# Kernel tuning notes

Measured on AMD Instinct MI355X. Metric: run time of the kernel, lower is better.

## Reference

```python
import jax, jax.numpy as jnp
import numpy as np

N, D, H, E, K, C = 8192, 1024, 2048, 8, 2, 2560  # tokens, d_model, hidden, experts, top_k, capacity


def setup_inputs() -> dict:
    key = jax.random.key(0)
    ks = jax.random.split(key, 8)
    s_in, s_h = 1.0 / np.sqrt(D), 1.0 / np.sqrt(H)
    return {
        "x": jax.random.normal(ks[0], (N, D), jnp.float32),
        "Wg": jax.random.uniform(ks[1], (D, E), jnp.float32, -s_in, s_in),
        "bg": jnp.zeros((E,), jnp.float32),
        "W1": jax.random.uniform(ks[2], (E, D, H), jnp.float32, -s_in, s_in),
        "b1": jnp.zeros((E, H), jnp.float32),
        "W2": jax.random.uniform(ks[3], (E, H, H), jnp.float32, -s_h, s_h),
        "b2": jnp.zeros((E, H), jnp.float32),
    }


def reference(x, Wg, bg, W1, b1, W2, b2):
    n = x.shape[0]
    logits = x @ Wg + bg                                  # [N, E]
    probs = jax.nn.softmax(logits, axis=-1)
    topk_probs, topk_idx = jax.lax.top_k(probs, K)        # [N, K]

    # auxiliary losses (training mode)
    importance = probs.sum(0)
    importance_loss = jnp.var(importance) / (E ** 2)
    rows = jnp.arange(n)[:, None]
    mask = jnp.zeros_like(probs).at[rows, topk_idx].set(1.0)
    routing_probs = probs * mask
    expert_usage = mask.mean(0)
    routing_weights = routing_probs.mean(0)
    load_balance_loss = E * (expert_usage * routing_weights).sum()
    aux_loss = importance_loss + load_balance_loss

    # dispatch: rank of each (token, k) slot within its expert, in flat order
    flat_e = topk_idx.reshape(-1)                          # [N*K]
    flat_p = topk_probs.reshape(-1)                        # [N*K]
    sample_idx = jnp.repeat(jnp.arange(n), K)              # [N*K]
    oh = (flat_e[:, None] == jnp.arange(E)[None, :]).astype(jnp.int32)  # [N*K, E]
    rank = jnp.take_along_axis(jnp.cumsum(oh, axis=0), flat_e[:, None], axis=1)[:, 0] - 1
    keep = rank < C                                        # capacity truncation (first-come)
    r_safe = jnp.where(keep, rank, C)                      # C is out-of-bounds -> dropped

    buf = jnp.zeros((E, C, D), x.dtype).at[flat_e, r_safe].set(x[sample_idx], mode="drop")
    h = jax.nn.gelu(jnp.einsum("ecd,edh->ech", buf, W1) + b1[:, None, :], approximate=False)
    y = jnp.einsum("ech,eho->eco", h, W2) + b2[:, None, :]  # [E, C, H]

    gathered = y[flat_e, jnp.minimum(r_safe, C - 1)]       # [N*K, H]
    weighted = gathered * (flat_p * keep.astype(x.dtype))[:, None]
    outputs = jnp.zeros((n, H), x.dtype).at[sample_idx].add(weighted)
    return outputs, aux_loss
```

## Files before the change

### kernel.cpp

```cpp
#include <hip/hip_runtime.h>
#include <math.h>
#include <stdint.h>

#define N_TOK 8192
#define DMODEL 1024
#define HID 2048
#define NEXP 8
#define TOPK 2
#define CAP 2560
#define NTALL 1408

typedef __bf16 bf16x8 __attribute__((ext_vector_type(8)));
typedef float f32x4 __attribute__((ext_vector_type(4)));
typedef unsigned int u32x4 __attribute__((ext_vector_type(4)));

__device__ __forceinline__ unsigned short f2b(float f) {
    unsigned int u = __builtin_bit_cast(unsigned int, f);
    u += 0x7fffu + ((u >> 16) & 1u);
    return (unsigned short)(u >> 16);
}
__device__ __forceinline__ float b2f(unsigned short s) {
    unsigned int u = ((unsigned int)s) << 16;
    return __builtin_bit_cast(float, u);
}

__device__ __forceinline__ float gelu_f(float v) {
    const float ax = fabsf(v) * 0.70710678118654752440f;
    const float t = __builtin_amdgcn_rcpf(1.f + 0.3275911f * ax);
    float poly = ((((1.061405429f * t - 1.453152027f) * t + 1.421413741f) * t
                   - 0.284496736f) * t + 0.254829592f) * t;
    float er = 1.f - poly * __expf(-ax * ax);
    er = (v >= 0.f) ? er : -er;
    return 0.5f * v * (1.f + er);
}

__device__ __forceinline__ void gload_lds16(const void* g, void* lds) {
    __builtin_amdgcn_global_load_lds(
        (const __attribute__((address_space(1))) unsigned int*)(uintptr_t)g,
        (__attribute__((address_space(3))) unsigned int*)(unsigned int)(uintptr_t)lds,
        16, 0, 0);
}

__global__ __launch_bounds__(256) void gate_kernel(
    const float* __restrict__ x, const float* __restrict__ Wg,
    const float* __restrict__ bg,
    int* __restrict__ flat_e, float* __restrict__ flat_p,
    float* __restrict__ imp_part, float* __restrict__ sel_part,
    unsigned short* __restrict__ xbf)
{
    __shared__ float s_imp[4][NEXP];
    __shared__ float s_sel[4][NEXP];
    const int wave = threadIdx.x >> 6;
    const int lane = threadIdx.x & 63;
    const int t = blockIdx.x * 4 + wave;

    float acc[NEXP];
#pragma unroll
    for (int e = 0; e < NEXP; ++e) acc[e] = 0.f;
    const float* xr = x + (size_t)t * DMODEL;
    unsigned short* xbr = xbf + (size_t)t * DMODEL;
    for (int d = lane; d < DMODEL; d += 64) {
        const float xv = xr[d];
        xbr[d] = f2b(xv);
#pragma unroll
        for (int e = 0; e < NEXP; ++e) acc[e] += xv * Wg[d * NEXP + e];
    }
#pragma unroll
    for (int off = 32; off > 0; off >>= 1) {
#pragma unroll
        for (int e = 0; e < NEXP; ++e) acc[e] += __shfl_xor(acc[e], off);
    }
    float lg[NEXP], mx = -1e30f;
#pragma unroll
    for (int e = 0; e < NEXP; ++e) { lg[e] = acc[e] + bg[e]; mx = fmaxf(mx, lg[e]); }
    float p[NEXP], s = 0.f;
#pragma unroll
    for (int e = 0; e < NEXP; ++e) { p[e] = expf(lg[e] - mx); s += p[e]; }
    const float inv = 1.f / s;
#pragma unroll
    for (int e = 0; e < NEXP; ++e) p[e] *= inv;

    int i0 = 0;
#pragma unroll
    for (int e = 1; e < NEXP; ++e) if (p[e] > p[i0]) i0 = e;
    int i1 = (i0 == 0) ? 1 : 0;
#pragma unroll
    for (int e = 0; e < NEXP; ++e) if (e != i0 && p[e] > p[i1]) i1 = e;

    if (lane == 0) {
        flat_e[2 * t] = i0;  flat_e[2 * t + 1] = i1;
        flat_p[2 * t] = p[i0]; flat_p[2 * t + 1] = p[i1];
#pragma unroll
        for (int e = 0; e < NEXP; ++e) {
            s_imp[wave][e] = p[e];
            s_sel[wave][e] = (e == i0) ? p[i0] : ((e == i1) ? p[i1] : 0.f);
        }
    }
    __syncthreads();
    if (threadIdx.x < NEXP) {
        const int e = threadIdx.x;
        float a = 0.f, b = 0.f;
#pragma unroll
        for (int w = 0; w < 4; ++w) { a += s_imp[w][e]; b += s_sel[w][e]; }
        imp_part[blockIdx.x * NEXP + e] = a;
        sel_part[blockIdx.x * NEXP + e] = b;
    }
}

__global__ __launch_bounds__(1024) void scan_kernel(
    const int* __restrict__ flat_e, int* __restrict__ slot_rank,
    int* __restrict__ row_token, int* __restrict__ n_kept,
    int* __restrict__ cnt_full, unsigned short* __restrict__ xbf_pad,
    int* __restrict__ ctrs)
{
    __shared__ int wave_tot[16][NEXP];
    __shared__ int base[NEXP];
    const int tid = threadIdx.x, lane = tid & 63, w = tid >> 6;
    if (tid < NEXP) base[tid] = 0;
    if (tid < 209) ctrs[tid] = 0;
    for (int i = tid; i < DMODEL; i += 1024) xbf_pad[i] = 0;
    __syncthreads();
    const unsigned long long ltmask =
        (lane == 0) ? 0ull : (~0ull >> (64 - lane));
    for (int chunk = 0; chunk < (N_TOK * TOPK) / 1024; ++chunk) {
        const int s = chunk * 1024 + tid;
        const int e = flat_e[s];
        int prefix = 0;
#pragma unroll
        for (int ee = 0; ee < NEXP; ++ee) {
            unsigned long long m = __ballot(e == ee);
            if (ee == e) prefix = __popcll(m & ltmask);
            if (lane == 0) wave_tot[w][ee] = __popcll(m);
        }
        __syncthreads();
        int before = base[e];
        for (int ww = 0; ww < w; ++ww) before += wave_tot[ww][e];
        const int rank = before + prefix;
        slot_rank[s] = rank;
        if (rank < CAP) row_token[e * CAP + rank] = s >> 1;
        __syncthreads();
        if (tid < NEXP) {
            int add = 0;
#pragma unroll
            for (int ww = 0; ww < 16; ++ww) add += wave_tot[ww][tid];
            base[tid] += add;
        }
        __syncthreads();
    }
    for (int i = tid; i < NEXP * CAP; i += 1024) {
        const int ee = i / CAP;
        const int r = i - ee * CAP;
        const int ne = base[ee] < CAP ? base[ee] : CAP;
        if (r >= ne) row_token[i] = N_TOK;
    }
    if (tid < NEXP) {
        n_kept[tid] = min(base[tid], CAP);
        cnt_full[tid] = base[tid];
    }
}

#define VMGATE4() do { asm volatile("s_waitcnt vmcnt(4)" ::: "memory"); \
                       __builtin_amdgcn_sched_barrier(0); } while (0)
#define VMGATE0() do { asm volatile("s_waitcnt vmcnt(0)" ::: "memory"); \
                       __builtin_amdgcn_sched_barrier(0); } while (0)
#define NOGATE() ((void)0)

#define PHASE(mf0, STAGE_STMT, TAIL_STMT) do {                                   \
    bf16x8 a0 = lda(c, (mf0), 0), a1 = lda(c, (mf0), 1);                         \
    bf16x8 a2 = lda(c, (mf0) + 1, 0), a3 = lda(c, (mf0) + 1, 1);                 \
    STAGE_STMT;                                                                  \
    __builtin_amdgcn_s_barrier();                                                \
    asm volatile("s_waitcnt lgkmcnt(0)" ::: "memory");                           \
    __builtin_amdgcn_sched_barrier(0);                                           \
    __builtin_amdgcn_s_setprio(1);                                               \
    _Pragma("unroll")                                                            \
    for (int nf = 0; nf < 4; ++nf) {                                             \
        acc[(mf0)][nf] = __builtin_amdgcn_mfma_f32_16x16x32_bf16(                \
            a0, bfr[nf][0], acc[(mf0)][nf], 0, 0, 0);                            \
        acc[(mf0)][nf] = __builtin_amdgcn_mfma_f32_16x16x32_bf16(                \
            a1, bfr[nf][1], acc[(mf0)][nf], 0, 0, 0);                            \
        acc[(mf0) + 1][nf] = __builtin_amdgcn_mfma_f32_16x16x32_bf16(            \
            a2, bfr[nf][0], acc[(mf0) + 1][nf], 0, 0, 0);                        \
        acc[(mf0) + 1][nf] = __builtin_amdgcn_mfma_f32_16x16x32_bf16(            \
            a3, bfr[nf][1], acc[(mf0) + 1][nf], 0, 0, 0);                        \
    }                                                                            \
    __builtin_amdgcn_s_setprio(0);                                               \
    TAIL_STMT;                                                                   \
    __builtin_amdgcn_s_barrier();                                                \
} while (0)

__global__ __launch_bounds__(512, 1) void mfma_fused(
    const unsigned short* __restrict__ xbf,
    const float* __restrict__ W1,
    const float* __restrict__ W2,
    unsigned short* w1t,
    unsigned short* w2t,
    const float* __restrict__ b1, const float* __restrict__ b2,
    unsigned short* hbuf,
    unsigned short* __restrict__ ybuf,
    const int* __restrict__ row_token, const int* __restrict__ n_kept,
    int* __restrict__ ctr)
{
    __shared__ unsigned short smem[81920];
    int* s_item = (int*)((char*)smem + 163836);
    int* hdone  = ctr + 1;
    int* w1flag = ctr + 81;
    int* w2flag = ctr + 145;

    const int t = threadIdx.x;
    const int w = t >> 6, lane = t & 63;
    const int wm = w >> 2, wn = w & 3;
    const int l15 = lane & 15, lq = lane >> 4;
    const int srow_lo = t >> 3;

    const int sx = (l15 & 4) << 3;
    const int kbx0 = (lq * 16) ^ sx;
    const int kbx1 = (64 + lq * 16) ^ sx;
    auto lda = [&](int cbuf, int mf, int ks) -> bf16x8 {
        return *(const bf16x8*)((const char*)smem + cbuf * 32768 +
                                (wm * 128 + mf * 16 + l15) * 128 + (ks ? kbx1 : kbx0));
    };
    auto ldb = [&](int cbuf, int nf, int ks) -> bf16x8 {
        return *(const bf16x8*)((const char*)smem + 65536 + cbuf * 32768 +
                                (wn * 64 + nf * 16 + l15) * 128 + (ks ? kbx1 : kbx0));
    };

    for (;;) {
        __syncthreads();
        if (t == 0) *s_item = atomicAdd(ctr, 1);
        __syncthreads();
        const int item = *s_item;
        if (item >= NTALL) break;

        bool isT = false, isW2 = false;
        int tIdx = 0, gIdx = 0;
        bool g2 = false;
        if (item < 64)        { isT = true; isW2 = false; tIdx = item; }
        else if (item < 128)  { gIdx = item - 64;  g2 = false; }
        else if (item < 192)  { isT = true; isW2 = true; tIdx = item - 128; }
        else if (item < 768)  { gIdx = item - 128; g2 = false; }
        else                  { gIdx = item - 768; g2 = true; }

        if (isT) {
            const int e = tIdx >> 3, n = tIdx & 7;
            const int R = isW2 ? HID : DMODEL;
            const float* Wsrc = (isW2 ? W2 : W1) + (size_t)e * R * HID + n * 256;
            unsigned short* Wdst =
                (isW2 ? w2t : w1t) + ((size_t)e * HID + n * 256) * R;
            unsigned short (*ts)[66] = (unsigned short(*)[66])smem;
            const int lr = t >> 6, lc = t & 63;
            const int cc = t >> 3, rq = (t & 7) * 8;
            for (int kb = 0; kb < R; kb += 64) {
                for (int nb = 0; nb < 4; ++nb) {
                    __syncthreads();
#pragma unroll
                    for (int i = 0; i < 8; ++i)
                        ts[lr + i * 8][lc] = f2b(__builtin_nontemporal_load(
                            &Wsrc[(size_t)(kb + lr + i * 8) * HID + nb * 64 + lc]));
                    __syncthreads();
                    unsigned short v[8];
#pragma unroll
                    for (int k2 = 0; k2 < 8; ++k2) v[k2] = ts[rq + k2][cc];
                    u32x4 o;
                    o[0] = v[0] | ((unsigned)v[1] << 16);
                    o[1] = v[2] | ((unsigned)v[3] << 16);
                    o[2] = v[4] | ((unsigned)v[5] << 16);
                    o[3] = v[6] | ((unsigned)v[7] << 16);
                    *(u32x4*)&Wdst[(size_t)(nb * 64 + cc) * R + kb + rq] = o;
                }
            }
            __syncthreads();
            if (t == 0)
                __hip_atomic_fetch_add(&(isW2 ? w2flag : w1flag)[tIdx], 1,
                                       __ATOMIC_RELEASE, __HIP_MEMORY_SCOPE_AGENT);
            continue;
        }

        const int e = gIdx / 80;
        const int rem = gIdx - e * 80;
        const int m = rem % 10;
        const int n = rem / 10;
        const int m0 = m * 256, n0 = n * 256;
        if (m0 >= n_kept[e]) continue;

        if (t == 0) {
            int* wf = g2 ? &w2flag[e * 8 + n] : &w1flag[e * 8 + n];
            while (__hip_atomic_load(wf, __ATOMIC_ACQUIRE,
                                     __HIP_MEMORY_SCOPE_AGENT) < 1)
                __builtin_amdgcn_s_sleep(8);
            if (g2) {
                while (__hip_atomic_load(&hdone[e * 10 + m], __ATOMIC_ACQUIRE,
                                         __HIP_MEMORY_SCOPE_AGENT) < 8)
                    __builtin_amdgcn_s_sleep(8);
            }
        }
        __syncthreads();

        const int Kdim = g2 ? HID : DMODEL;
        const int NT = Kdim >> 6;
        const unsigned short* A  = g2 ? hbuf : xbf;
        const unsigned short* Wt = g2 ? w2t : w1t;

        long abase[2][2], bbase[2][2];
#pragma unroll
        for (int h = 0; h < 2; ++h) {
#pragma unroll
            for (int cc2 = 0; cc2 < 2; ++cc2) {
                const int srow = h * 128 + cc2 * 64 + srow_lo;
                const int skoff = ((t & 7) * 8) ^ ((srow & 4) << 2);
                long ar;
                if (g2) ar = ((long)e * CAP + m0 + srow) * (long)Kdim;
                else    ar = (long)row_token[e * CAP + m0 + srow] * Kdim;
                abase[h][cc2] = ar + skoff;
                bbase[h][cc2] = ((long)e * HID + n0 + srow) * (long)Kdim + skoff;
            }
        }
        auto stageA = [&](int buf, int h0, int ktile) {
            const long ko = (long)ktile * 64;
            char* base = (char*)smem + buf * 32768 + h0 * 16384 + w * 1024;
            gload_lds16(A + (h0 ? abase[1][0] : abase[0][0]) + ko, base);
            gload_lds16(A + (h0 ? abase[1][1] : abase[0][1]) + ko, base + 8192);
        };
        auto stageB = [&](int buf, int h0, int ktile) {
            const long ko = (long)ktile * 64;
            char* base = (char*)smem + 65536 + buf * 32768 + h0 * 16384 + w * 1024;
            gload_lds16(Wt + (h0 ? bbase[1][0] : bbase[0][0]) + ko, base);
            gload_lds16(Wt + (h0 ? bbase[1][1] : bbase[0][1]) + ko, base + 8192);
        };

        f32x4 acc[8][4];
#pragma unroll
        for (int mm = 0; mm < 8; ++mm)
#pragma unroll
            for (int nn = 0; nn < 4; ++nn) acc[mm][nn] = (f32x4)0.f;

        stageA(0, 0, 0); stageA(0, 1, 0);
        stageB(0, 0, 0); stageB(0, 1, 0);
        stageB(1, 0, 1); stageB(1, 1, 1);
        VMGATE4();
        __builtin_amdgcn_s_barrier();

        int bcur = 0;
        for (int kt = 0; kt < NT; ++kt) {
            const int c = kt & 1, o = c ^ 1;
            const int ktA = kt + 1;
            const int ktB = kt + 2;
            int bst = bcur + 2; if (bst >= 3) bst -= 3;

            bf16x8 bfr[4][2];
#pragma unroll
            for (int nf = 0; nf < 4; ++nf) {
                bfr[nf][0] = ldb(bcur, nf, 0);
                bfr[nf][1] = ldb(bcur, nf, 1);
            }
            PHASE(0, if (ktA < NT) stageA(o, 0, ktA), NOGATE());
            PHASE(2, if (ktA < NT) stageA(o, 1, ktA), NOGATE());
            PHASE(4, if (ktB < NT) stageB(bst, 0, ktB), NOGATE());
            if (ktB < NT) {
                PHASE(6, stageB(bst, 1, ktB), VMGATE4());
            } else {
                PHASE(6, NOGATE(), VMGATE0());
            }
            bcur = (bcur == 2) ? 0 : bcur + 1;
        }

        const float* be = (g2 ? b2 : b1) + (size_t)e * HID;
        unsigned short* outp = g2 ? ybuf : hbuf;
        float bv[4];
#pragma unroll
        for (int nf = 0; nf < 4; ++nf)
            bv[nf] = be[n0 + wn * 64 + nf * 16 + l15];
#pragma unroll
        for (int mf = 0; mf < 8; ++mf) {
#pragma unroll
            for (int j = 0; j < 4; ++j) {
                const int row = m0 + wm * 128 + mf * 16 + lq * 4 + j;
                unsigned short* orow =
                    outp + ((size_t)e * CAP + row) * HID + n0 + wn * 64 + l15;
#pragma unroll
                for (int nf = 0; nf < 4; ++nf) {
                    float v = acc[mf][nf][j] + bv[nf];
                    if (!g2) {
                        v = gelu_f(v);
                        orow[nf * 16] = f2b(v);
                    } else {
                        __builtin_nontemporal_store(f2b(v), &orow[nf * 16]);
                    }
                }
            }
        }

        if (!g2) {
            __syncthreads();
            if (t == 0)
                __hip_atomic_fetch_add(&hdone[e * 10 + m], 1, __ATOMIC_RELEASE,
                                       __HIP_MEMORY_SCOPE_AGENT);
        }
    }
}

__global__ __launch_bounds__(256) void combine_kernel(
    const unsigned short* __restrict__ y, const int* __restrict__ flat_e,
    const float* __restrict__ flat_p, const int* __restrict__ slot_rank,
    float* __restrict__ out)
{
    const int t = blockIdx.x;
    const int e0 = flat_e[2 * t], e1 = flat_e[2 * t + 1];
    const int r0 = slot_rank[2 * t], r1 = slot_rank[2 * t + 1];
    const bool k0 = r0 < CAP, k1 = r1 < CAP;
    const float w0 = k0 ? flat_p[2 * t] : 0.f;
    const float w1 = k1 ? flat_p[2 * t + 1] : 0.f;
    const unsigned short* y0 = y + ((size_t)e0 * CAP + (k0 ? r0 : 0)) * HID;
    const unsigned short* y1 = y + ((size_t)e1 * CAP + (k1 ? r1 : 0)) * HID;
    float* orow = out + (size_t)t * HID;
    const int c = threadIdx.x * 8;
    u32x4 av = k0 ? __builtin_nontemporal_load((const u32x4*)(y0 + c)) : (u32x4)0u;
    u32x4 bv = k1 ? __builtin_nontemporal_load((const u32x4*)(y1 + c)) : (u32x4)0u;
    float o[8];
    auto comb2 = [&](unsigned int a, unsigned int b, float* dst) {
        dst[0] = w0 * b2f((unsigned short)(a & 0xffffu)) +
                 w1 * b2f((unsigned short)(b & 0xffffu));
        dst[1] = w0 * b2f((unsigned short)(a >> 16)) +
                 w1 * b2f((unsigned short)(b >> 16));
    };
    comb2(av[0], bv[0], o + 0); comb2(av[1], bv[1], o + 2);
    comb2(av[2], bv[2], o + 4); comb2(av[3], bv[3], o + 6);
    f32x4 o0 = {o[0], o[1], o[2], o[3]};
    f32x4 o1 = {o[4], o[5], o[6], o[7]};
    __builtin_nontemporal_store(o0, (f32x4*)(orow + c));
    __builtin_nontemporal_store(o1, (f32x4*)(orow + c + 4));
}

__global__ __launch_bounds__(64) void aux_kernel(
    const float* __restrict__ imp_part, const float* __restrict__ sel_part,
    const int* __restrict__ cnt_full, float* __restrict__ out_aux,
    const int nparts)
{
    const int lane = threadIdx.x;
    __shared__ float imp_s[NEXP], sel_s[NEXP];
    for (int e = 0; e < NEXP; ++e) {
        float a = 0.f, b = 0.f;
        for (int i = lane; i < nparts; i += 64) {
            a += imp_part[i * NEXP + e];
            b += sel_part[i * NEXP + e];
        }
#pragma unroll
        for (int off = 32; off > 0; off >>= 1) {
            a += __shfl_xor(a, off);
            b += __shfl_xor(b, off);
        }
        if (lane == 0) { imp_s[e] = a; sel_s[e] = b; }
    }
    __syncthreads();
    if (lane == 0) {
        double mean = 0.0;
        for (int e = 0; e < NEXP; ++e) mean += imp_s[e];
        mean /= NEXP;
        double var = 0.0;
        for (int e = 0; e < NEXP; ++e) {
            const double d = (double)imp_s[e] - mean;
            var += d * d;
        }
        var /= NEXP;
        double load = 0.0;
        for (int e = 0; e < NEXP; ++e)
            load += ((double)cnt_full[e] / N_TOK) * ((double)sel_s[e] / N_TOK);
        load *= NEXP;
        out_aux[0] = (float)(var / (NEXP * NEXP) + load);
    }
}

extern "C" void kernel_launch(void* const* d_in, const int* in_sizes, int n_in,
                              void* d_out, int out_size, void* d_ws, size_t ws_size,
                              hipStream_t stream) {
    const float* x  = (const float*)d_in[0];
    const float* Wg = (const float*)d_in[1];
    const float* bg = (const float*)d_in[2];
    const float* W1 = (const float*)d_in[3];
    const float* b1 = (const float*)d_in[4];
    const float* W2 = (const float*)d_in[5];
    const float* b2 = (const float*)d_in[6];
    float* out = (float*)d_out;
    (void)in_sizes; (void)n_in; (void)out_size; (void)ws_size;

    char* ws = (char*)d_ws;
    size_t off = 0;
    auto alloc = [&](size_t bytes) -> void* {
        void* p = ws + off;
        off = (off + bytes + 255) & ~(size_t)255;
        return p;
    };
    int*   n_kept    = (int*)alloc(NEXP * sizeof(int));
    int*   cnt_full  = (int*)alloc(NEXP * sizeof(int));
    int*   ctrs      = (int*)alloc(209 * sizeof(int));
    int*   flat_e    = (int*)alloc((size_t)N_TOK * TOPK * sizeof(int));
    float* flat_p    = (float*)alloc((size_t)N_TOK * TOPK * sizeof(float));
    int*   slot_rank = (int*)alloc((size_t)N_TOK * TOPK * sizeof(int));
    int*   row_tok   = (int*)alloc((size_t)NEXP * CAP * sizeof(int));
    float* imp_part  = (float*)alloc((size_t)(N_TOK / 4) * NEXP * sizeof(float));
    float* sel_part  = (float*)alloc((size_t)(N_TOK / 4) * NEXP * sizeof(float));
    unsigned short* xbf  = (unsigned short*)alloc((size_t)(N_TOK + 1) * DMODEL * 2);
    unsigned short* w1t  = (unsigned short*)alloc((size_t)NEXP * DMODEL * HID * 2);
    unsigned short* w2t  = (unsigned short*)alloc((size_t)NEXP * HID * HID * 2);
    unsigned short* hbuf = (unsigned short*)alloc((size_t)NEXP * CAP * HID * 2);
    unsigned short* ybuf = (unsigned short*)alloc((size_t)NEXP * CAP * HID * 2);

    gate_kernel<<<N_TOK / 4, 256, 0, stream>>>(x, Wg, bg, flat_e, flat_p,
                                               imp_part, sel_part, xbf);
    scan_kernel<<<1, 1024, 0, stream>>>(flat_e, slot_rank, row_tok, n_kept,
                                        cnt_full, xbf + (size_t)N_TOK * DMODEL,
                                        ctrs);

    mfma_fused<<<256, 512, 0, stream>>>(xbf, W1, W2, w1t, w2t, b1, b2,
                                        hbuf, ybuf, row_tok, n_kept, ctrs);

    combine_kernel<<<N_TOK, 256, 0, stream>>>(ybuf, flat_e, flat_p, slot_rank, out);
    aux_kernel<<<1, 64, 0, stream>>>(imp_part, sel_part, cnt_full,
                                     out + (size_t)N_TOK * HID, N_TOK / 4);
}
```

Measured before the change: 526.7 us.

## Move W1 transpose-convert into a separate kernel before the fused GEMM

The W1 fp32-to-bf16 transpose now runs in a dedicated grid-wide kernel instead of as work items inside the persistent fused GEMM kernel. GEMM1 items no longer spin on per-tile W1 flags, and the work-item list and counter array shrink to match. The W2 transpose stays in-kernel and is still overlapped with GEMM1. The trade is an extra launch plus a serial dependency, in exchange for a fully parallel transpose and no per-tile polling. The final output stores also switch from nontemporal to normal stores.

```diff
diff --git a/kernel.cpp b/kernel.cpp
--- a/kernel.cpp
+++ b/kernel.cpp
@@ -8,7 +8,7 @@
 #define NEXP 8
 #define TOPK 2
 #define CAP 2560
-#define NTALL 1408
+#define NTALL 1344
 
 typedef __bf16 bf16x8 __attribute__((ext_vector_type(8)));
 typedef float f32x4 __attribute__((ext_vector_type(4)));
@@ -117,7 +117,7 @@
     __shared__ int base[NEXP];
     const int tid = threadIdx.x, lane = tid & 63, w = tid >> 6;
     if (tid < NEXP) base[tid] = 0;
-    if (tid < 209) ctrs[tid] = 0;
+    if (tid < 145) ctrs[tid] = 0;
     for (int i = tid; i < DMODEL; i += 1024) xbf_pad[i] = 0;
     __syncthreads();
     const unsigned long long ltmask =
@@ -156,6 +156,37 @@
     if (tid < NEXP) {
         n_kept[tid] = min(base[tid], CAP);
         cnt_full[tid] = base[tid];
+    }
+}
+
+__global__ __launch_bounds__(256) void transpose_cvt(
+    const float* __restrict__ W, unsigned short* __restrict__ Wt,
+    const int R, const int Cdim)
+{
+    __shared__ unsigned short s[64][66];
+    const int e = blockIdx.z;
+    const int c0 = blockIdx.x * 64, r0 = blockIdx.y * 64;
+    const float* We = W + (size_t)e * R * Cdim;
+    unsigned short* Wte = Wt + (size_t)e * R * Cdim;
+    const int tid = threadIdx.x;
+    const int lr = tid >> 6;
+    const int lc = tid & 63;
+#pragma unroll
+    for (int i = 0; i < 16; ++i)
+        s[lr + i * 4][lc] =
+            f2b(__builtin_nontemporal_load(&We[(size_t)(r0 + lr + i * 4) * Cdim + c0 + lc]));
+    __syncthreads();
+#pragma unroll
+    for (int pass = 0; pass < 2; ++pass) {
+        const int cc = (tid >> 3) + pass * 32;
+        const int rq = (tid & 7) * 8;
+        unsigned short v[8];
+#pragma unroll
+        for (int k = 0; k < 8; ++k) v[k] = s[rq + k][cc];
+        u32x4 o;
+        o[0] = v[0] | ((unsigned)v[1] << 16); o[1] = v[2] | ((unsigned)v[3] << 16);
+        o[2] = v[4] | ((unsigned)v[5] << 16); o[3] = v[6] | ((unsigned)v[7] << 16);
+        *(u32x4*)&Wte[(size_t)(c0 + cc) * R + r0 + rq] = o;
     }
 }
 
@@ -191,9 +222,8 @@
 
 __global__ __launch_bounds__(512, 1) void mfma_fused(
     const unsigned short* __restrict__ xbf,
-    const float* __restrict__ W1,
     const float* __restrict__ W2,
-    unsigned short* w1t,
+    const unsigned short* __restrict__ w1t,
     unsigned short* w2t,
     const float* __restrict__ b1, const float* __restrict__ b2,
     unsigned short* hbuf,
@@ -204,8 +234,7 @@
     __shared__ unsigned short smem[81920];
     int* s_item = (int*)((char*)smem + 163836);
     int* hdone  = ctr + 1;
-    int* w1flag = ctr + 81;
-    int* w2flag = ctr + 145;
+    int* w2flag = ctr + 81;
 
     const int t = threadIdx.x;
     const int w = t >> 6, lane = t & 63;
@@ -232,25 +261,18 @@
         const int item = *s_item;
         if (item >= NTALL) break;
 
-        bool isT = false, isW2 = false;
-        int tIdx = 0, gIdx = 0;
         bool g2 = false;
-        if (item < 64)        { isT = true; isW2 = false; tIdx = item; }
-        else if (item < 128)  { gIdx = item - 64;  g2 = false; }
-        else if (item < 192)  { isT = true; isW2 = true; tIdx = item - 128; }
-        else if (item < 768)  { gIdx = item - 128; g2 = false; }
-        else                  { gIdx = item - 768; g2 = true; }
-
-        if (isT) {
+        int gIdx = 0;
+        if (item < 64)        { gIdx = item; }
+        else if (item < 128)  {
+            const int tIdx = item - 64;
             const int e = tIdx >> 3, n = tIdx & 7;
-            const int R = isW2 ? HID : DMODEL;
-            const float* Wsrc = (isW2 ? W2 : W1) + (size_t)e * R * HID + n * 256;
-            unsigned short* Wdst =
-                (isW2 ? w2t : w1t) + ((size_t)e * HID + n * 256) * R;
+            const float* Wsrc = W2 + (size_t)e * HID * HID + n * 256;
+            unsigned short* Wdst = w2t + ((size_t)e * HID + n * 256) * HID;
             unsigned short (*ts)[66] = (unsigned short(*)[66])smem;
             const int lr = t >> 6, lc = t & 63;
             const int cc = t >> 3, rq = (t & 7) * 8;
-            for (int kb = 0; kb < R; kb += 64) {
+            for (int kb = 0; kb < HID; kb += 64) {
                 for (int nb = 0; nb < 4; ++nb) {
                     __syncthreads();
 #pragma unroll
@@ -266,15 +288,17 @@
                     o[1] = v[2] | ((unsigned)v[3] << 16);
                     o[2] = v[4] | ((unsigned)v[5] << 16);
                     o[3] = v[6] | ((unsigned)v[7] << 16);
-                    *(u32x4*)&Wdst[(size_t)(nb * 64 + cc) * R + kb + rq] = o;
+                    *(u32x4*)&Wdst[(size_t)(nb * 64 + cc) * HID + kb + rq] = o;
                 }
             }
             __syncthreads();
             if (t == 0)
-                __hip_atomic_fetch_add(&(isW2 ? w2flag : w1flag)[tIdx], 1,
-                                       __ATOMIC_RELEASE, __HIP_MEMORY_SCOPE_AGENT);
+                __hip_atomic_fetch_add(&w2flag[tIdx], 1, __ATOMIC_RELEASE,
+                                       __HIP_MEMORY_SCOPE_AGENT);
             continue;
         }
+        else if (item < 704)  { gIdx = item - 64; }
+        else                  { gIdx = item - 704; g2 = true; }
 
         const int e = gIdx / 80;
         const int rem = gIdx - e * 80;
@@ -283,18 +307,17 @@
         const int m0 = m * 256, n0 = n * 256;
         if (m0 >= n_kept[e]) continue;
 
-        if (t == 0) {
-            int* wf = g2 ? &w2flag[e * 8 + n] : &w1flag[e * 8 + n];
-            while (__hip_atomic_load(wf, __ATOMIC_ACQUIRE,
-                                     __HIP_MEMORY_SCOPE_AGENT) < 1)
-                __builtin_amdgcn_s_sleep(8);
-            if (g2) {
+        if (g2) {
+            if (t == 0) {
+                while (__hip_atomic_load(&w2flag[e * 8 + n], __ATOMIC_ACQUIRE,
+                                         __HIP_MEMORY_SCOPE_AGENT) < 1)
+                    __builtin_amdgcn_s_sleep(8);
                 while (__hip_atomic_load(&hdone[e * 10 + m], __ATOMIC_ACQUIRE,
                                          __HIP_MEMORY_SCOPE_AGENT) < 8)
                     __builtin_amdgcn_s_sleep(8);
             }
-        }
-        __syncthreads();
+            __syncthreads();
+        }
 
         const int Kdim = g2 ? HID : DMODEL;
         const int NT = Kdim >> 6;
@@ -380,12 +403,8 @@
 #pragma unroll
                 for (int nf = 0; nf < 4; ++nf) {
                     float v = acc[mf][nf][j] + bv[nf];
-                    if (!g2) {
-                        v = gelu_f(v);
-                        orow[nf * 16] = f2b(v);
-                    } else {
-                        __builtin_nontemporal_store(f2b(v), &orow[nf * 16]);
-                    }
+                    if (!g2) v = gelu_f(v);
+                    orow[nf * 16] = f2b(v);
                 }
             }
         }
@@ -492,7 +511,7 @@
     };
     int*   n_kept    = (int*)alloc(NEXP * sizeof(int));
     int*   cnt_full  = (int*)alloc(NEXP * sizeof(int));
-    int*   ctrs      = (int*)alloc(209 * sizeof(int));
+    int*   ctrs      = (int*)alloc(145 * sizeof(int));
     int*   flat_e    = (int*)alloc((size_t)N_TOK * TOPK * sizeof(int));
     float* flat_p    = (float*)alloc((size_t)N_TOK * TOPK * sizeof(float));
     int*   slot_rank = (int*)alloc((size_t)N_TOK * TOPK * sizeof(int));
@@ -511,7 +530,9 @@
                                         cnt_full, xbf + (size_t)N_TOK * DMODEL,
                                         ctrs);
 
-    mfma_fused<<<256, 512, 0, stream>>>(xbf, W1, W2, w1t, w2t, b1, b2,
+    transpose_cvt<<<dim3(HID / 64, DMODEL / 64, NEXP), 256, 0, stream>>>(W1, w1t, DMODEL, HID);
+
+    mfma_fused<<<256, 512, 0, stream>>>(xbf, W2, w1t, w2t, b1, b2,
                                         hbuf, ybuf, row_tok, n_kept, ctrs);
 
     combine_kernel<<<N_TOK, 256, 0, stream>>>(ybuf, flat_e, flat_p, slot_rank, out);
```

Measured after the change: 541.2 us. 1.03x slower.
